# Kernel optimization log

Measured on AMD Instinct MI355X. Metric: run time of the kernel, lower is better.

Reference implementation:

```python
import jax, jax.numpy as jnp
import numpy as np

B, S, D_MODEL = 2, 1024, 512
HEAD = 8
DEPTH = D_MODEL // HEAD  # 64
NFEAT = 64


def _make_orf(rng, n_features, depth):
    # Mirrors OrthogonalRandomFeature: QR of uniform blocks, scaled by norms of gaussian rows.
    n, rem = divmod(n_features, depth)
    blocks = []
    for _ in range(n):
        q, _ = np.linalg.qr(rng.random((depth, depth)))
        blocks.append(q)
    if rem > 0:
        q, _ = np.linalg.qr(rng.random((depth, depth)))
        blocks.append(q[:rem])
    orf = np.concatenate(blocks, axis=0)
    mult = np.linalg.norm(rng.standard_normal((n_features, depth)), axis=1)
    return jnp.asarray(mult[:, None] * orf, dtype=jnp.float32)


def setup_inputs() -> dict:
    key = jax.random.key(0)
    ks = jax.random.split(key, 12)
    rng = np.random.default_rng(0)
    scale = 0.02
    inp = {
        "query": jax.random.normal(ks[0], (B, S, D_MODEL), dtype=jnp.float32),
        "key": jax.random.normal(ks[1], (B, S, D_MODEL), dtype=jnp.float32),
        "value": jax.random.normal(ks[2], (B, S, D_MODEL), dtype=jnp.float32),
        "Wq": jax.random.normal(ks[3], (DEPTH, DEPTH), dtype=jnp.float32) * scale,
        "bq": jnp.zeros((DEPTH,), dtype=jnp.float32),
        "Wk": jax.random.normal(ks[4], (DEPTH, DEPTH), dtype=jnp.float32) * scale,
        "bk": jnp.zeros((DEPTH,), dtype=jnp.float32),
        "Wv": jax.random.normal(ks[5], (DEPTH, DEPTH), dtype=jnp.float32) * scale,
        "bv": jnp.zeros((DEPTH,), dtype=jnp.float32),
        "orf_q": _make_orf(rng, NFEAT, DEPTH),
        "orf_k": _make_orf(rng, NFEAT, DEPTH),
        "Wfc": jax.random.normal(ks[6], (D_MODEL, D_MODEL), dtype=jnp.float32) * scale,
        "bfc": jnp.zeros((D_MODEL,), dtype=jnp.float32),
        "causal": 1,
    }
    return inp


def _kernel_fn(x, orf):
    # x: [n,h,s,d], orf: [f,d]; normalization uses ORF.shape[-1] = depth
    norm = 1.0 / (orf.shape[-1] ** 0.25)
    out = jnp.einsum('nhsd,fd->nhsf', x * norm, orf)
    return jax.nn.relu(out) + 0.001


def _causal_attention(q, k, v):
    # q,k: [n,h,s,f]; v: [n,h,s,d]
    k_cumsum = jnp.cumsum(k, axis=-2)                    # [n,h,s,f]
    x = jnp.einsum('nhkf,nhkd->nhkfd', k, v)             # [n,h,s,f,d]
    x = jnp.cumsum(x, axis=-3)
    x = x / k_cumsum[..., None]
    return jnp.einsum('nhqfd,nhqf->nhqd', x, q)          # [n,h,s,d]


def _bidirectional_attention(q, k, v):
    kt_i = jnp.sum(k, axis=-2)                           # [n,h,f]
    norm = 1.0 / jnp.einsum('nhqf,nhf->nhq', q, kt_i)    # [n,h,s]
    k_v = jnp.einsum('nhkf,nhkd->nhfd', k, v)            # [n,h,f,d]
    return jnp.einsum('nhfd,nhqf,nhq->nhqd', k_v, q, norm)


def reference(query, key, value, Wq, bq, Wk, bk, Wv, bv, orf_q, orf_k, Wfc, bfc, causal):
    b, s, _ = query.shape
    depth = Wq.shape[0]
    head = query.shape[-1] // depth
    # [b,s,d_model] -> [b,h,s,depth]
    q = query.reshape(b, s, head, depth).transpose(0, 2, 1, 3)
    k = key.reshape(b, s, head, depth).transpose(0, 2, 1, 3)
    v = value.reshape(b, s, head, depth).transpose(0, 2, 1, 3)
    # per-head Linear on depth (torch: x @ W.T + b)
    q = jnp.einsum('nhsd,ed->nhse', q, Wq) + bq
    k = jnp.einsum('nhsd,ed->nhse', k, Wk) + bk
    v = jnp.einsum('nhsd,ed->nhse', v, Wv) + bv
    q = _kernel_fn(q, orf_q)
    k = _kernel_fn(k, orf_k)
    if causal:
        out = _causal_attention(q, k, v)
    else:
        out = _bidirectional_attention(q, k, v)
    out = out.transpose(0, 2, 1, 3).reshape(b, s, head * depth)
    return jnp.einsum('nse,oe->nso', out, Wfc) + bfc
```

## Files before the change

kernel.cpp:

```cpp
#include <hip/hip_runtime.h>


#define SS 1024
#define HH 8
#define DD 64
#define FF 64
#define DM 512
#define NCH 16

typedef __bf16 bf16_t;
typedef __attribute__((ext_vector_type(8))) __bf16 bf16x8;
typedef __attribute__((ext_vector_type(4))) __bf16 bf16x4;
typedef __attribute__((ext_vector_type(4))) float f32x4;

#define MFMA16(a,b,c) __builtin_amdgcn_mfma_f32_16x16x32_bf16((a),(b),(c),0,0,0)

__device__ inline bf16x8 cvt_f32x8(const float* p){
    const float4* p4 = (const float4*)p;
    float4 x = p4[0], y = p4[1];
    bf16x8 r;
    r[0]=(__bf16)x.x; r[1]=(__bf16)x.y; r[2]=(__bf16)x.z; r[3]=(__bf16)x.w;
    r[4]=(__bf16)y.x; r[5]=(__bf16)y.y; r[6]=(__bf16)y.z; r[7]=(__bf16)y.w;
    return r;
}

__global__ __launch_bounds__(256) void kfuse(
    const float* __restrict__ orf_q, const float* __restrict__ orf_k,
    const float* __restrict__ Wq, const float* __restrict__ bq,
    const float* __restrict__ Wk, const float* __restrict__ bk,
    const float* __restrict__ Wv, const float* __restrict__ Wfc,
    bf16_t* __restrict__ Mtq, bf16_t* __restrict__ Mtk,
    float* __restrict__ cq, float* __restrict__ ck,
    bf16_t* __restrict__ WvB, bf16_t* __restrict__ WfcB)
{
    const int tid = threadIdx.x, bid = blockIdx.x;
    if (bid < 2) {
        const float* ORF = bid ? orf_k : orf_q;
        const float* W   = bid ? Wk : Wq;
        const float* bb  = bid ? bk : bq;
        bf16_t* Mt = bid ? Mtk : Mtq;
        float* cc  = bid ? ck : cq;
        const float norm = 0.35355339059327373f;
        const int f = tid >> 2, d0 = (tid & 3) * 16;
        float acc[16];
        #pragma unroll
        for (int j=0;j<16;j++) acc[j]=0.f;
        float bacc = 0.f;
        for (int e=0;e<64;e++){
            float oe = ORF[f*64+e];
            const float* wr = W + e*64 + d0;
            #pragma unroll
            for (int j=0;j<16;j++) acc[j] += oe*wr[j];
            bacc += oe*bb[e];
        }
        #pragma unroll
        for (int j=0;j<16;j++) Mt[f*64+d0+j] = (__bf16)(norm*acc[j]);
        if ((tid&3)==0) cc[f] = norm*bacc;
    } else if (bid == 2) {
        for (int i=tid;i<4096;i+=256) WvB[i] = (__bf16)Wv[i];
    } else {
        const float4* W4 = (const float4*)Wfc;
        for (int i=(bid-3)*256+tid; i<65536; i+=13*256){
            float4 v = W4[i];
            bf16x4 o; o[0]=(__bf16)v.x; o[1]=(__bf16)v.y; o[2]=(__bf16)v.z; o[3]=(__bf16)v.w;
            *(bf16x4*)(WfcB + 4*i) = o;
        }
    }
}

__global__ __launch_bounds__(512) void kproj(
    const float* __restrict__ q_in, const float* __restrict__ k_in,
    const float* __restrict__ v_in,
    const bf16_t* __restrict__ Mtq, const float* __restrict__ cq,
    const bf16_t* __restrict__ Mtk, const float* __restrict__ ck,
    const bf16_t* __restrict__ WvB, const float* __restrict__ bv,
    bf16_t* __restrict__ PHI_Q, bf16_t* __restrict__ PHI_K,
    bf16_t* __restrict__ PHI_KT, bf16_t* __restrict__ VPT,
    float* __restrict__ CST, float* __restrict__ KCS)
{
    __shared__ bf16_t kt[64*72];
    __shared__ bf16_t vt[64*72];
    __shared__ float dsT[64*68];
    __shared__ float part[256];
    const int tid = threadIdx.x;
    const int l = tid & 63;
    const int w = __builtin_amdgcn_readfirstlane(tid >> 6);
    const int ww = w & 3;
    const int qd = l >> 4, m = l & 15;
    const int bid = blockIdx.x;
    const int bh = bid >> 4, ch = bid & 15;
    const int b = bh >> 3, h = bh & 7;
    const int s0 = ch*64;
    const int sw = s0 + ww*16;

    if (w < 4) {
        const float* xp = q_in + ((size_t)(b*SS + sw + m))*DM + h*DD;
        bf16x8 a0 = cvt_f32x8(xp + qd*8);
        bf16x8 a1 = cvt_f32x8(xp + 32 + qd*8);
        #pragma unroll
        for (int nt=0;nt<4;nt++){
            const int f = nt*16 + m;
            float cb = cq[f];
            f32x4 acc = {cb,cb,cb,cb};
            acc = MFMA16(a0, *(const bf16x8*)(Mtq + f*64 + qd*8), acc);
            acc = MFMA16(a1, *(const bf16x8*)(Mtq + f*64 + 32 + qd*8), acc);
            #pragma unroll
            for (int r=0;r<4;r++){
                float v = acc[r];
                v = (v>0.f)?v:0.f; v += 0.001f;
                PHI_Q[((size_t)bh*SS + sw + qd*4 + r)*FF + f] = (__bf16)v;
            }
        }
    } else {
        const float* xp = k_in + ((size_t)(b*SS + sw + m))*DM + h*DD;
        bf16x8 a0 = cvt_f32x8(xp + qd*8);
        bf16x8 a1 = cvt_f32x8(xp + 32 + qd*8);
        #pragma unroll
        for (int nt=0;nt<4;nt++){
            const int f = nt*16 + m;
            float cb = ck[f];
            f32x4 acc = {cb,cb,cb,cb};
            acc = MFMA16(a0, *(const bf16x8*)(Mtk + f*64 + qd*8), acc);
            acc = MFMA16(a1, *(const bf16x8*)(Mtk + f*64 + 32 + qd*8), acc);
            #pragma unroll
            for (int r=0;r<4;r++){
                float v = acc[r];
                v = (v>0.f)?v:0.f; v += 0.001f;
                __bf16 h16 = (__bf16)v;
                PHI_K[((size_t)bh*SS + sw + qd*4 + r)*FF + f] = h16;
                kt[f*72 + ww*16 + qd*4 + r] = h16;
            }
        }
    }
    __syncthreads();

    if (tid < 256) {
        const int f = tid >> 2, sg = tid & 3;
        bf16x8 v0 = *(bf16x8*)&kt[f*72 + sg*16];
        bf16x8 v1 = *(bf16x8*)&kt[f*72 + sg*16 + 8];
        bf16_t* dst = PHI_KT + ((size_t)bh*64 + f)*SS + s0 + sg*16;
        *(bf16x8*)dst = v0; *(bf16x8*)(dst+8) = v1;
    } else {
        const float* xp = v_in + ((size_t)(b*SS + sw + m))*DM + h*DD;
        bf16x8 a0 = cvt_f32x8(xp + qd*8);
        bf16x8 a1 = cvt_f32x8(xp + 32 + qd*8);
        #pragma unroll
        for (int nt=0;nt<4;nt++){
            const int e = nt*16 + m;
            float cb = bv[e];
            f32x4 acc = {cb,cb,cb,cb};
            acc = MFMA16(a0, *(const bf16x8*)(WvB + e*64 + qd*8), acc);
            acc = MFMA16(a1, *(const bf16x8*)(WvB + e*64 + 32 + qd*8), acc);
            #pragma unroll
            for (int r=0;r<4;r++)
                vt[e*72 + ww*16 + qd*4 + r] = (__bf16)acc[r];
        }
    }
    __syncthreads();

    {
        const int ft = ww, np = (w >> 2) * 2;
        bf16x8 a0 = *(bf16x8*)&kt[(ft*16+m)*72 + qd*8];
        bf16x8 a1 = *(bf16x8*)&kt[(ft*16+m)*72 + 32 + qd*8];
        #pragma unroll
        for (int j=0;j<2;j++){
            const int nt = np + j;
            f32x4 acc = {0.f,0.f,0.f,0.f};
            acc = MFMA16(a0, *(bf16x8*)&vt[(nt*16+m)*72 + qd*8], acc);
            acc = MFMA16(a1, *(bf16x8*)&vt[(nt*16+m)*72 + 32 + qd*8], acc);
            #pragma unroll
            for (int r=0;r<4;r++)
                dsT[(nt*16+m)*68 + ft*16 + qd*4 + r] = acc[r];
        }
    }
    if (tid < 256) {
        const int d = tid >> 2, sg = tid & 3;
        bf16x8 v0 = *(bf16x8*)&vt[d*72 + sg*16];
        bf16x8 v1 = *(bf16x8*)&vt[d*72 + sg*16 + 8];
        bf16_t* dst = VPT + ((size_t)bh*64 + d)*SS + s0 + sg*16;
        *(bf16x8*)dst = v0; *(bf16x8*)(dst+8) = v1;
    } else {
        const int t2 = tid - 256;
        const int f = t2 & 63, sg = t2 >> 6;
        bf16x8 x0 = *(bf16x8*)&kt[f*72 + sg*16];
        bf16x8 x1 = *(bf16x8*)&kt[f*72 + sg*16 + 8];
        float sm = 0.f;
        #pragma unroll
        for (int j=0;j<8;j++) sm += (float)x0[j] + (float)x1[j];
        part[sg*64 + f] = sm;
    }
    __syncthreads();

    if (tid < 256) {
        const int d = tid >> 2, F = (tid & 3) * 16;
        float* dst = CST + ((size_t)bid*64 + d)*64 + F;
        #pragma unroll
        for (int j=0;j<4;j++)
            *(float4*)(dst + 4*j) = *(float4*)&dsT[d*68 + F + 4*j];
    } else if (tid < 320) {
        const int f = tid - 256;
        KCS[(size_t)bid*64 + f] = part[f] + part[64+f] + part[128+f] + part[192+f];
    }
}

__global__ __launch_bounds__(512) void kattn(
    const bf16_t* __restrict__ PHI_Q, const bf16_t* __restrict__ PHI_K,
    const bf16_t* __restrict__ PHI_KT, const bf16_t* __restrict__ VPT,
    const float* __restrict__ CST, const float* __restrict__ KCS,
    bf16_t* __restrict__ O)
{
    __shared__ float kct[64*67];
    __shared__ bf16_t qnl[64*72];
    __shared__ bf16_t sAl[64*72];
    __shared__ bf16_t pT[64*72];
    __shared__ float scanp[256];
    __shared__ float kcsp[64];
    const int tid = threadIdx.x;
    const int l = tid & 63;
    const int w = __builtin_amdgcn_readfirstlane(tid >> 6);
    const int rt = w & 3;
    const int np = (w >> 2) * 2;
    const int qd = l >> 4, m = l & 15;
    const int bid = blockIdx.x;
    const int bh = bid >> 4, ch = bid & 15;
    const int cs0 = ch*64;

    if (tid >= 256) {
        const int t2 = tid - 256;
        const int base = t2 * 16;
        const int d = t2 >> 2, f0 = (t2 & 3) * 16;
        float acc[16];
        #pragma unroll
        for (int j=0;j<16;j++) acc[j]=0.f;
        for (int cc = 0; cc < ch; cc++) {
            const float4* p = (const float4*)(CST + ((size_t)(bh*NCH + cc))*4096 + base);
            #pragma unroll
            for (int j=0;j<4;j++){
                float4 t = p[j];
                acc[4*j]+=t.x; acc[4*j+1]+=t.y; acc[4*j+2]+=t.z; acc[4*j+3]+=t.w;
            }
        }
        bf16x8 o0, o1;
        #pragma unroll
        for (int j=0;j<8;j++){ o0[j]=(__bf16)acc[j]; o1[j]=(__bf16)acc[8+j]; }
        *(bf16x8*)&pT[d*72 + f0]     = o0;
        *(bf16x8*)&pT[d*72 + f0 + 8] = o1;
    } else {
        const int f = tid >> 2, sg = tid & 3;
        const bf16_t* kp = PHI_KT + ((size_t)bh*64 + f)*SS + cs0 + sg*16;
        bf16x8 x0 = *(const bf16x8*)kp;
        bf16x8 x1 = *(const bf16x8*)(kp+8);
        #pragma unroll
        for (int j=0;j<8;j++){
            kct[f*67 + sg*16 + j]     = (float)x0[j];
            kct[f*67 + sg*16 + 8 + j] = (float)x1[j];
        }
        if (tid < 64) {
            float r = 0.f;
            for (int cc = 0; cc < ch; cc++) r += KCS[((size_t)(bh*NCH + cc))*64 + tid];
            kcsp[tid] = r;
        }
    }
    __syncthreads();

    const int f2 = tid >> 2, sg2 = tid & 3;
    float v16[16];
    if (tid < 256) {
        #pragma unroll
        for (int j=0;j<16;j++) v16[j] = kct[f2*67 + sg2*16 + j];
        #pragma unroll
        for (int j=1;j<16;j++) v16[j] += v16[j-1];
        scanp[f2*4 + sg2] = v16[15];
    }
    __syncthreads();
    if (tid < 256) {
        float offs = kcsp[f2];
        if (sg2 > 0) offs += scanp[f2*4 + 0];
        if (sg2 > 1) offs += scanp[f2*4 + 1];
        if (sg2 > 2) offs += scanp[f2*4 + 2];
        #pragma unroll
        for (int j=0;j<16;j++) kct[f2*67 + sg2*16 + j] = offs + v16[j];
    }
    __syncthreads();

    if (tid < 256) {
        const int sr = tid >> 2, F = (tid & 3) * 16;
        const bf16_t* qp = PHI_Q + ((size_t)bh*SS + cs0 + sr)*FF + F;
        bf16x8 x0 = *(const bf16x8*)qp;
        bf16x8 x1 = *(const bf16x8*)(qp+8);
        bf16x8 o0, o1;
        #pragma unroll
        for (int j=0;j<8;j++){
            o0[j] = (__bf16)((float)x0[j] / kct[(F+j)*67 + sr]);
            o1[j] = (__bf16)((float)x1[j] / kct[(F+8+j)*67 + sr]);
        }
        *(bf16x8*)&qnl[sr*72 + F]     = o0;
        *(bf16x8*)&qnl[sr*72 + F + 8] = o1;
    }
    __syncthreads();

    bf16x8 qa0 = *(bf16x8*)&qnl[(rt*16+m)*72 + qd*8];
    bf16x8 qa1 = *(bf16x8*)&qnl[(rt*16+m)*72 + 32 + qd*8];

    #pragma unroll
    for (int j=0;j<2;j++){
        const int nt = np + j;
        const bf16_t* kb = PHI_K + ((size_t)bh*SS + cs0 + nt*16 + m)*FF;
        f32x4 acc = {0.f,0.f,0.f,0.f};
        acc = MFMA16(qa0, *(const bf16x8*)(kb + qd*8), acc);
        acc = MFMA16(qa1, *(const bf16x8*)(kb + 32 + qd*8), acc);
        const int t_loc = nt*16 + m;
        #pragma unroll
        for (int r=0;r<4;r++){
            const int s_loc = rt*16 + qd*4 + r;
            float v = (t_loc <= s_loc) ? acc[r] : 0.f;
            sAl[s_loc*72 + t_loc] = (__bf16)v;
        }
    }
    __syncthreads();

    bf16x8 sa0 = *(bf16x8*)&sAl[(rt*16+m)*72 + qd*8];
    bf16x8 sa1 = *(bf16x8*)&sAl[(rt*16+m)*72 + 32 + qd*8];

    #pragma unroll
    for (int j=0;j<2;j++){
        const int nt = np + j;
        const int d = nt*16 + m;
        const bf16_t* vb = VPT + ((size_t)bh*64 + d)*SS + cs0;
        f32x4 acc = {0.f,0.f,0.f,0.f};
        acc = MFMA16(sa0, *(const bf16x8*)(vb + qd*8), acc);
        acc = MFMA16(sa1, *(const bf16x8*)(vb + 32 + qd*8), acc);
        acc = MFMA16(qa0, *(const bf16x8*)&pT[d*72 + qd*8], acc);
        acc = MFMA16(qa1, *(const bf16x8*)&pT[d*72 + 32 + qd*8], acc);
        #pragma unroll
        for (int r=0;r<4;r++)
            O[((size_t)bh*SS + cs0 + rt*16 + qd*4 + r)*DD + d] = (__bf16)acc[r];
    }
}

__global__ __launch_bounds__(512) void kfc(
    const bf16_t* __restrict__ O, const bf16_t* __restrict__ WfcB,
    const float* __restrict__ bfc, float* __restrict__ out)
{
    const int tid = threadIdx.x;
    const int l = tid & 63;
    const int w = __builtin_amdgcn_readfirstlane(tid >> 6);
    const int rw = w & 3, cpair = (w >> 2) * 2;
    const int qd = l >> 4, m = l & 15;
    const int bid = blockIdx.x;
    const int rb = bid >> 3, cb = bid & 7;
    const int r0 = rb*64 + rw*16;

    f32x4 acc[2];
    #pragma unroll
    for (int j=0;j<2;j++){
        float bb = bfc[cb*64 + (cpair+j)*16 + m];
        acc[j][0]=bb; acc[j][1]=bb; acc[j][2]=bb; acc[j][3]=bb;
    }
    const int row = r0 + m;
    const int b = row >> 10, s = row & 1023;
    #pragma unroll 4
    for (int c=0;c<16;c++){
        const int h = c >> 1;
        const int doff = (c & 1)*32 + qd*8;
        bf16x8 a = *(const bf16x8*)(O + ((size_t)((b*HH + h)*SS + s))*DD + doff);
        #pragma unroll
        for (int j=0;j<2;j++){
            bf16x8 bfr = *(const bf16x8*)(WfcB + (size_t)(cb*64 + (cpair+j)*16 + m)*DM + c*32 + qd*8);
            acc[j] = MFMA16(a, bfr, acc[j]);
        }
    }
    #pragma unroll
    for (int j=0;j<2;j++){
        #pragma unroll
        for (int r=0;r<4;r++){
            const int rr = r0 + qd*4 + r;
            out[(size_t)rr*DM + cb*64 + (cpair+j)*16 + m] = acc[j][r];
        }
    }
}

extern "C" void kernel_launch(void* const* d_in, const int* in_sizes, int n_in,
                              void* d_out, int out_size, void* d_ws, size_t ws_size,
                              hipStream_t stream) {
    const float* q_in  = (const float*)d_in[0];
    const float* k_in  = (const float*)d_in[1];
    const float* v_in  = (const float*)d_in[2];
    const float* Wq    = (const float*)d_in[3];
    const float* bq    = (const float*)d_in[4];
    const float* Wk    = (const float*)d_in[5];
    const float* bk    = (const float*)d_in[6];
    const float* Wv    = (const float*)d_in[7];
    const float* bv    = (const float*)d_in[8];
    const float* orf_q = (const float*)d_in[9];
    const float* orf_k = (const float*)d_in[10];
    const float* Wfc   = (const float*)d_in[11];
    const float* bfc   = (const float*)d_in[12];

    float* CST   = (float*)d_ws;
    float* KCS   = CST + 1048576;
    float* cq    = KCS + 16384;
    float* ck    = cq + 64;
    bf16_t* PHI_Q  = (bf16_t*)(ck + 64);
    bf16_t* PHI_K  = PHI_Q + 1048576;
    bf16_t* PHI_KT = PHI_K + 1048576;
    bf16_t* VPT    = PHI_KT + 1048576;
    bf16_t* O      = VPT + 1048576;
    bf16_t* Mtq    = O + 1048576;
    bf16_t* Mtk    = Mtq + 4096;
    bf16_t* WvB    = Mtk + 4096;
    bf16_t* WfcB   = WvB + 4096;

    kfuse<<<16, 256, 0, stream>>>(orf_q, orf_k, Wq, bq, Wk, bk, Wv, Wfc,
                                  Mtq, Mtk, cq, ck, WvB, WfcB);
    kproj<<<256, 512, 0, stream>>>(q_in, k_in, v_in, Mtq, cq, Mtk, ck, WvB, bv,
                                   PHI_Q, PHI_K, PHI_KT, VPT, CST, KCS);
    kattn<<<256, 512, 0, stream>>>(PHI_Q, PHI_K, PHI_KT, VPT, CST, KCS, O);
    kfc<<<256, 512, 0, stream>>>(O, WfcB, bfc, (float*)d_out);
}
```

Before: 133.2 us.

## Fold weight-prep kernel into projection kernel with redundant per-block recompute

Removes the separate kfuse launch by having every kproj block recompute the ORF·W fused matrices, biases and bf16 Wv into shared memory, and convert its own slice of Wfc to bf16. Activation loads for q/k/v are issued before this prep so their latency overlaps with it. This drops one kernel launch and its dependency gap, but each of the 256 blocks now runs a 64x64x64 fp32 matmul for both q and k and reads the small weights repeatedly, which adds per-block latency before the MFMA work starts.

```diff
diff --git a/kernel.cpp b/kernel.cpp
--- a/kernel.cpp
+++ b/kernel.cpp
@@ -15,69 +15,30 @@
 
 #define MFMA16(a,b,c) __builtin_amdgcn_mfma_f32_16x16x32_bf16((a),(b),(c),0,0,0)
 
-__device__ inline bf16x8 cvt_f32x8(const float* p){
-    const float4* p4 = (const float4*)p;
-    float4 x = p4[0], y = p4[1];
+__device__ inline bf16x8 pack8(float4 x, float4 y){
     bf16x8 r;
     r[0]=(__bf16)x.x; r[1]=(__bf16)x.y; r[2]=(__bf16)x.z; r[3]=(__bf16)x.w;
     r[4]=(__bf16)y.x; r[5]=(__bf16)y.y; r[6]=(__bf16)y.z; r[7]=(__bf16)y.w;
     return r;
 }
 
-__global__ __launch_bounds__(256) void kfuse(
-    const float* __restrict__ orf_q, const float* __restrict__ orf_k,
-    const float* __restrict__ Wq, const float* __restrict__ bq,
-    const float* __restrict__ Wk, const float* __restrict__ bk,
-    const float* __restrict__ Wv, const float* __restrict__ Wfc,
-    bf16_t* __restrict__ Mtq, bf16_t* __restrict__ Mtk,
-    float* __restrict__ cq, float* __restrict__ ck,
-    bf16_t* __restrict__ WvB, bf16_t* __restrict__ WfcB)
-{
-    const int tid = threadIdx.x, bid = blockIdx.x;
-    if (bid < 2) {
-        const float* ORF = bid ? orf_k : orf_q;
-        const float* W   = bid ? Wk : Wq;
-        const float* bb  = bid ? bk : bq;
-        bf16_t* Mt = bid ? Mtk : Mtq;
-        float* cc  = bid ? ck : cq;
-        const float norm = 0.35355339059327373f;
-        const int f = tid >> 2, d0 = (tid & 3) * 16;
-        float acc[16];
-        #pragma unroll
-        for (int j=0;j<16;j++) acc[j]=0.f;
-        float bacc = 0.f;
-        for (int e=0;e<64;e++){
-            float oe = ORF[f*64+e];
-            const float* wr = W + e*64 + d0;
-            #pragma unroll
-            for (int j=0;j<16;j++) acc[j] += oe*wr[j];
-            bacc += oe*bb[e];
-        }
-        #pragma unroll
-        for (int j=0;j<16;j++) Mt[f*64+d0+j] = (__bf16)(norm*acc[j]);
-        if ((tid&3)==0) cc[f] = norm*bacc;
-    } else if (bid == 2) {
-        for (int i=tid;i<4096;i+=256) WvB[i] = (__bf16)Wv[i];
-    } else {
-        const float4* W4 = (const float4*)Wfc;
-        for (int i=(bid-3)*256+tid; i<65536; i+=13*256){
-            float4 v = W4[i];
-            bf16x4 o; o[0]=(__bf16)v.x; o[1]=(__bf16)v.y; o[2]=(__bf16)v.z; o[3]=(__bf16)v.w;
-            *(bf16x4*)(WfcB + 4*i) = o;
-        }
-    }
-}
-
 __global__ __launch_bounds__(512) void kproj(
     const float* __restrict__ q_in, const float* __restrict__ k_in,
     const float* __restrict__ v_in,
-    const bf16_t* __restrict__ Mtq, const float* __restrict__ cq,
-    const bf16_t* __restrict__ Mtk, const float* __restrict__ ck,
-    const bf16_t* __restrict__ WvB, const float* __restrict__ bv,
+    const float* __restrict__ Wq, const float* __restrict__ bq,
+    const float* __restrict__ Wk, const float* __restrict__ bk,
+    const float* __restrict__ Wv, const float* __restrict__ bv,
+    const float* __restrict__ orf_q, const float* __restrict__ orf_k,
+    const float* __restrict__ Wfc,
     bf16_t* __restrict__ PHI_Q, bf16_t* __restrict__ PHI_K,
     bf16_t* __restrict__ PHI_KT, bf16_t* __restrict__ VPT,
-    float* __restrict__ CST, float* __restrict__ KCS)
+    float* __restrict__ CST, float* __restrict__ KCS,
+    bf16_t* __restrict__ WfcB)
 {
+    __shared__ bf16_t Mtq_l[64*72];
+    __shared__ bf16_t Mtk_l[64*72];
+    __shared__ bf16_t WvB_l[64*72];
+    __shared__ float cql[64], ckl[64];
     __shared__ bf16_t kt[64*72];
     __shared__ bf16_t vt[64*72];
     __shared__ float dsT[64*68];
@@ -93,42 +54,97 @@
     const int s0 = ch*64;
     const int sw = s0 + ww*16;
 
-    if (w < 4) {
-        const float* xp = q_in + ((size_t)(b*SS + sw + m))*DM + h*DD;
-        bf16x8 a0 = cvt_f32x8(xp + qd*8);
-        bf16x8 a1 = cvt_f32x8(xp + 32 + qd*8);
-        #pragma unroll
-        for (int nt=0;nt<4;nt++){
-            const int f = nt*16 + m;
-            float cb = cq[f];
-            f32x4 acc = {cb,cb,cb,cb};
-            acc = MFMA16(a0, *(const bf16x8*)(Mtq + f*64 + qd*8), acc);
-            acc = MFMA16(a1, *(const bf16x8*)(Mtq + f*64 + 32 + qd*8), acc);
-            #pragma unroll
-            for (int r=0;r<4;r++){
-                float v = acc[r];
-                v = (v>0.f)?v:0.f; v += 0.001f;
-                PHI_Q[((size_t)bh*SS + sw + qd*4 + r)*FF + f] = (__bf16)v;
+    const float* xrow = ((w < 4) ? q_in : k_in) + ((size_t)(b*SS + sw + m))*DM + h*DD;
+    float4 pA0 = *(const float4*)(xrow + qd*8);
+    float4 pA1 = *(const float4*)(xrow + qd*8 + 4);
+    float4 pB0 = *(const float4*)(xrow + 32 + qd*8);
+    float4 pB1 = *(const float4*)(xrow + 32 + qd*8 + 4);
+    float4 vA0 = {0,0,0,0}, vA1 = {0,0,0,0}, vB0 = {0,0,0,0}, vB1 = {0,0,0,0};
+    if (w >= 4){
+        const float* vrow = v_in + ((size_t)(b*SS + sw + m))*DM + h*DD;
+        vA0 = *(const float4*)(vrow + qd*8);
+        vA1 = *(const float4*)(vrow + qd*8 + 4);
+        vB0 = *(const float4*)(vrow + 32 + qd*8);
+        vB1 = *(const float4*)(vrow + 32 + qd*8 + 4);
+    }
+
+    {
+        const float norm = 0.35355339059327373f;
+        const int f = tid >> 3, d0 = (tid & 7) * 8;
+        float accq[8], acck[8];
+        #pragma unroll
+        for (int j=0;j<8;j++){ accq[j]=0.f; acck[j]=0.f; }
+        for (int e=0;e<64;e++){
+            float oq = orf_q[f*64+e];
+            float ok = orf_k[f*64+e];
+            const float* wq = Wq + e*64 + d0;
+            const float* wk = Wk + e*64 + d0;
+            #pragma unroll
+            for (int j=0;j<8;j++){ accq[j] += oq*wq[j]; acck[j] += ok*wk[j]; }
+        }
+        #pragma unroll
+        for (int j=0;j<8;j++){
+            Mtq_l[f*72 + d0 + j] = (__bf16)(norm*accq[j]);
+            Mtk_l[f*72 + d0 + j] = (__bf16)(norm*acck[j]);
+        }
+        if (tid < 64){
+            float bacc = 0.f;
+            for (int e=0;e<64;e++) bacc += orf_q[tid*64+e]*bq[e];
+            cql[tid] = norm*bacc;
+        } else if (tid < 128){
+            const int f2 = tid - 64;
+            float bacc = 0.f;
+            for (int e=0;e<64;e++) bacc += orf_k[f2*64+e]*bk[e];
+            ckl[f2] = norm*bacc;
+        }
+        #pragma unroll
+        for (int i=0;i<8;i++){
+            int idx = i*512 + tid;
+            WvB_l[(idx >> 6)*72 + (idx & 63)] = (__bf16)Wv[idx];
+        }
+        if (tid < 256){
+            const int idx = bid*256 + tid;
+            float4 v = ((const float4*)Wfc)[idx];
+            bf16x4 o; o[0]=(__bf16)v.x; o[1]=(__bf16)v.y; o[2]=(__bf16)v.z; o[3]=(__bf16)v.w;
+            *(bf16x4*)(WfcB + 4*idx) = o;
+        }
+    }
+    __syncthreads();
+
+    {
+        bf16x8 a0 = pack8(pA0, pA1);
+        bf16x8 a1 = pack8(pB0, pB1);
+        if (w < 4) {
+            #pragma unroll
+            for (int nt=0;nt<4;nt++){
+                const int f = nt*16 + m;
+                float cb = cql[f];
+                f32x4 acc = {cb,cb,cb,cb};
+                acc = MFMA16(a0, *(const bf16x8*)&Mtq_l[f*72 + qd*8], acc);
+                acc = MFMA16(a1, *(const bf16x8*)&Mtq_l[f*72 + 32 + qd*8], acc);
+                #pragma unroll
+                for (int r=0;r<4;r++){
+                    float v = acc[r];
+                    v = (v>0.f)?v:0.f; v += 0.001f;
+                    PHI_Q[((size_t)bh*SS + sw + qd*4 + r)*FF + f] = (__bf16)v;
+                }
             }
-        }
-    } else {
-        const float* xp = k_in + ((size_t)(b*SS + sw + m))*DM + h*DD;
-        bf16x8 a0 = cvt_f32x8(xp + qd*8);
-        bf16x8 a1 = cvt_f32x8(xp + 32 + qd*8);
-        #pragma unroll
-        for (int nt=0;nt<4;nt++){
-            const int f = nt*16 + m;
-            float cb = ck[f];
-            f32x4 acc = {cb,cb,cb,cb};
-            acc = MFMA16(a0, *(const bf16x8*)(Mtk + f*64 + qd*8), acc);
-            acc = MFMA16(a1, *(const bf16x8*)(Mtk + f*64 + 32 + qd*8), acc);
-            #pragma unroll
-            for (int r=0;r<4;r++){
-                float v = acc[r];
-                v = (v>0.f)?v:0.f; v += 0.001f;
-                __bf16 h16 = (__bf16)v;
-                PHI_K[((size_t)bh*SS + sw + qd*4 + r)*FF + f] = h16;
-                kt[f*72 + ww*16 + qd*4 + r] = h16;
+        } else {
+            #pragma unroll
+            for (int nt=0;nt<4;nt++){
+                const int f = nt*16 + m;
+                float cb = ckl[f];
+                f32x4 acc = {cb,cb,cb,cb};
+                acc = MFMA16(a0, *(const bf16x8*)&Mtk_l[f*72 + qd*8], acc);
+                acc = MFMA16(a1, *(const bf16x8*)&Mtk_l[f*72 + 32 + qd*8], acc);
+                #pragma unroll
+                for (int r=0;r<4;r++){
+                    float v = acc[r];
+                    v = (v>0.f)?v:0.f; v += 0.001f;
+                    __bf16 h16 = (__bf16)v;
+                    PHI_K[((size_t)bh*SS + sw + qd*4 + r)*FF + f] = h16;
+                    kt[f*72 + ww*16 + qd*4 + r] = h16;
+                }
             }
         }
     }
@@ -141,16 +157,15 @@
         bf16_t* dst = PHI_KT + ((size_t)bh*64 + f)*SS + s0 + sg*16;
         *(bf16x8*)dst = v0; *(bf16x8*)(dst+8) = v1;
     } else {
-        const float* xp = v_in + ((size_t)(b*SS + sw + m))*DM + h*DD;
-        bf16x8 a0 = cvt_f32x8(xp + qd*8);
-        bf16x8 a1 = cvt_f32x8(xp + 32 + qd*8);
+        bf16x8 a0 = pack8(vA0, vA1);
+        bf16x8 a1 = pack8(vB0, vB1);
         #pragma unroll
         for (int nt=0;nt<4;nt++){
             const int e = nt*16 + m;
             float cb = bv[e];
             f32x4 acc = {cb,cb,cb,cb};
-            acc = MFMA16(a0, *(const bf16x8*)(WvB + e*64 + qd*8), acc);
-            acc = MFMA16(a1, *(const bf16x8*)(WvB + e*64 + 32 + qd*8), acc);
+            acc = MFMA16(a0, *(const bf16x8*)&WvB_l[e*72 + qd*8], acc);
+            acc = MFMA16(a1, *(const bf16x8*)&WvB_l[e*72 + 32 + qd*8], acc);
             #pragma unroll
             for (int r=0;r<4;r++)
                 vt[e*72 + ww*16 + qd*4 + r] = (__bf16)acc[r];
@@ -399,22 +414,16 @@
 
     float* CST   = (float*)d_ws;
     float* KCS   = CST + 1048576;
-    float* cq    = KCS + 16384;
-    float* ck    = cq + 64;
-    bf16_t* PHI_Q  = (bf16_t*)(ck + 64);
+    bf16_t* PHI_Q  = (bf16_t*)(KCS + 16384);
     bf16_t* PHI_K  = PHI_Q + 1048576;
     bf16_t* PHI_KT = PHI_K + 1048576;
     bf16_t* VPT    = PHI_KT + 1048576;
     bf16_t* O      = VPT + 1048576;
-    bf16_t* Mtq    = O + 1048576;
-    bf16_t* Mtk    = Mtq + 4096;
-    bf16_t* WvB    = Mtk + 4096;
-    bf16_t* WfcB   = WvB + 4096;
-
-    kfuse<<<16, 256, 0, stream>>>(orf_q, orf_k, Wq, bq, Wk, bk, Wv, Wfc,
-                                  Mtq, Mtk, cq, ck, WvB, WfcB);
-    kproj<<<256, 512, 0, stream>>>(q_in, k_in, v_in, Mtq, cq, Mtk, ck, WvB, bv,
-                                   PHI_Q, PHI_K, PHI_KT, VPT, CST, KCS);
+    bf16_t* WfcB   = O + 1048576;
+
+    kproj<<<256, 512, 0, stream>>>(q_in, k_in, v_in, Wq, bq, Wk, bk, Wv, bv,
+                                   orf_q, orf_k, Wfc,
+                                   PHI_Q, PHI_K, PHI_KT, VPT, CST, KCS, WfcB);
     kattn<<<256, 512, 0, stream>>>(PHI_Q, PHI_K, PHI_KT, VPT, CST, KCS, O);
     kfc<<<256, 512, 0, stream>>>(O, WfcB, bfc, (float*)d_out);
 }
```

Measured after the change: 131.8 us. About the same (-1.1%).
